# Performance work log

Measured on AMD Instinct MI355X. Metric: run time of the kernel, lower is better.

Reference implementation:

```python
import jax, jax.numpy as jnp
import numpy as np


def setup_inputs() -> dict:
    key = jax.random.key(0)
    k1, k2 = jax.random.split(key)
    B, C = 8192, 4096
    y_hat = jax.random.normal(k1, (B, C), dtype=jnp.float32)
    y = jax.random.randint(k2, (B, C), 0, 2).astype(jnp.float32)
    return {"y_hat": y_hat, "y": y}


def _bce_with_logits(x, y):
    # numerically stable mean BCE-with-logits (matches torch reduction='mean')
    return jnp.mean(jnp.maximum(x, 0.0) - x * y + jnp.log1p(jnp.exp(-jnp.abs(x))))


def _cross_label_dependency(x, y):
    # per-row: sum_{j: y=0, k: y!=0} exp(x_j - x_k) / (n0 * n1)
    # factorized: (sum_neg exp(x_j)) * (sum_pos exp(-x_k)) / (n0 * n1)
    pos = (y != 0.0)
    neg = jnp.logical_not(pos)
    s_neg = jnp.sum(jnp.where(neg, jnp.exp(x), 0.0), axis=1)   # [B]
    s_pos = jnp.sum(jnp.where(pos, jnp.exp(-x), 0.0), axis=1)  # [B]
    n0 = jnp.sum(neg, axis=1).astype(x.dtype)
    n1 = jnp.sum(pos, axis=1).astype(x.dtype)
    denom = n0 * n1
    per_row = jnp.where(denom > 0, s_neg * s_pos / jnp.maximum(denom, 1.0), 0.0)
    return jnp.mean(per_row)


def reference(y_hat, y):
    return _bce_with_logits(y_hat, y) + _cross_label_dependency(y_hat, y)
```

## Files before the change

### kernel.cpp

```cpp
#include <hip/hip_runtime.h>

#define B_ROWS 8192
#define C_COLS 4096

__device__ __forceinline__ float wave_reduce_sum(float v) {
    #pragma unroll
    for (int o = 32; o > 0; o >>= 1) v += __shfl_down(v, o, 64);
    return v;
}

__global__ __launch_bounds__(256) void row_stage(const float* __restrict__ x,
                                                 const float* __restrict__ y,
                                                 float* __restrict__ row_out) {
    const int row = blockIdx.x;
    const size_t base = (size_t)row * C_COLS;
    const float4* x4 = reinterpret_cast<const float4*>(x + base);
    const float4* y4 = reinterpret_cast<const float4*>(y + base);

    const float LOG2E  = 1.44269504088896340736f;
    const float N2LOG2E = -2.0f * 1.44269504088896340736f;
    const float LN2    = 0.69314718055994530942f;

    float s_neg = 0.f, s_pos = 0.f, bce = 0.f, n1 = 0.f;

    #pragma unroll
    for (int it = 0; it < 4; ++it) {
        const int i = it * 256 + threadIdx.x;
        float4 xv = x4[i];
        float4 yv = y4[i];
        float xs[4] = {xv.x, xv.y, xv.z, xv.w};
        float ys[4] = {yv.x, yv.y, yv.z, yv.w};
        float prod = 1.0f;
        #pragma unroll
        for (int k = 0; k < 4; ++k) {
            float xx = xs[k];
            float yy = ys[k];
            float m  = fmaf(N2LOG2E, yy, LOG2E);
            float eu = __builtin_amdgcn_exp2f(xx * m);
            s_pos = fmaf(yy,        eu, s_pos);
            s_neg = fmaf(1.0f - yy, eu, s_neg);
            n1   += yy;
            prod  = fmaf(prod, eu, prod);
        }
        bce = fmaf(LN2, __builtin_amdgcn_logf(prod), bce);
    }

    float a = wave_reduce_sum(s_neg);
    float b = wave_reduce_sum(s_pos);
    float c = wave_reduce_sum(bce);
    float d = wave_reduce_sum(n1);

    __shared__ float red[4][4];
    const int lane = threadIdx.x & 63;
    const int wid  = threadIdx.x >> 6;
    if (lane == 0) {
        red[wid][0] = a; red[wid][1] = b; red[wid][2] = c; red[wid][3] = d;
    }
    __syncthreads();

    if (threadIdx.x == 0) {
        float SN = red[0][0] + red[1][0] + red[2][0] + red[3][0];
        float SP = red[0][1] + red[1][1] + red[2][1] + red[3][1];
        float BC = red[0][2] + red[1][2] + red[2][2] + red[3][2];
        float N1 = red[0][3] + red[1][3] + red[2][3] + red[3][3];
        float N0 = (float)C_COLS - N1;
        float denom = N0 * N1;
        float per_row = (denom > 0.f) ? (SN * SP) / denom : 0.f;
        row_out[row] = BC * (1.0f / ((float)B_ROWS * (float)C_COLS))
                     + per_row * (1.0f / (float)B_ROWS);
    }
}

__global__ __launch_bounds__(256) void final_reduce(const float* __restrict__ row_vals,
                                                    float* __restrict__ out) {
    float s = 0.f;
    for (int i = threadIdx.x; i < B_ROWS; i += 256) s += row_vals[i];
    s = wave_reduce_sum(s);
    __shared__ float red[4];
    const int lane = threadIdx.x & 63;
    const int wid  = threadIdx.x >> 6;
    if (lane == 0) red[wid] = s;
    __syncthreads();
    if (threadIdx.x == 0) out[0] = red[0] + red[1] + red[2] + red[3];
}

extern "C" void kernel_launch(void* const* d_in, const int* in_sizes, int n_in,
                              void* d_out, int out_size, void* d_ws, size_t ws_size,
                              hipStream_t stream) {
    const float* x = (const float*)d_in[0];
    const float* y = (const float*)d_in[1];
    float* out = (float*)d_out;
    float* row_vals = (float*)d_ws;

    row_stage<<<B_ROWS, 256, 0, stream>>>(x, y, row_vals);
    final_reduce<<<1, 256, 0, stream>>>(row_vals, out);
}
```

Measured before the change: 50.82 us.

## Fuse final reduction via atomicAdd and hoist row loads ahead of compute

```diff
diff --git a/kernel.cpp b/kernel.cpp
--- a/kernel.cpp
+++ b/kernel.cpp
@@ -2,6 +2,8 @@
 
 #define B_ROWS 8192
 #define C_COLS 4096
+
+typedef float fv4 __attribute__((ext_vector_type(4)));
 
 __device__ __forceinline__ float wave_reduce_sum(float v) {
     #pragma unroll
@@ -11,41 +13,44 @@
 
 __global__ __launch_bounds__(256) void row_stage(const float* __restrict__ x,
                                                  const float* __restrict__ y,
-                                                 float* __restrict__ row_out) {
+                                                 float* __restrict__ out) {
     const int row = blockIdx.x;
     const size_t base = (size_t)row * C_COLS;
-    const float4* x4 = reinterpret_cast<const float4*>(x + base);
-    const float4* y4 = reinterpret_cast<const float4*>(y + base);
+    const fv4* x4 = reinterpret_cast<const fv4*>(x + base);
+    const fv4* y4 = reinterpret_cast<const fv4*>(y + base);
 
-    const float LOG2E  = 1.44269504088896340736f;
+    const float LOG2E   = 1.44269504088896340736f;
     const float N2LOG2E = -2.0f * 1.44269504088896340736f;
-    const float LN2    = 0.69314718055994530942f;
+    const float LN2     = 0.69314718055994530942f;
 
-    float s_neg = 0.f, s_pos = 0.f, bce = 0.f, n1 = 0.f;
+    fv4 xr[4], yr[4];
+    #pragma unroll
+    for (int it = 0; it < 4; ++it) {
+        const int i = it * 256 + threadIdx.x;
+        xr[it] = x4[i];
+        yr[it] = __builtin_nontemporal_load(&y4[i]);
+    }
+
+    float s_all = 0.f, s_pos = 0.f, bce = 0.f, n1 = 0.f;
 
     #pragma unroll
     for (int it = 0; it < 4; ++it) {
-        const int i = it * 256 + threadIdx.x;
-        float4 xv = x4[i];
-        float4 yv = y4[i];
-        float xs[4] = {xv.x, xv.y, xv.z, xv.w};
-        float ys[4] = {yv.x, yv.y, yv.z, yv.w};
         float prod = 1.0f;
         #pragma unroll
         for (int k = 0; k < 4; ++k) {
-            float xx = xs[k];
-            float yy = ys[k];
+            float xx = xr[it][k];
+            float yy = yr[it][k];
             float m  = fmaf(N2LOG2E, yy, LOG2E);
             float eu = __builtin_amdgcn_exp2f(xx * m);
-            s_pos = fmaf(yy,        eu, s_pos);
-            s_neg = fmaf(1.0f - yy, eu, s_neg);
+            s_all = s_all + eu;
+            s_pos = fmaf(yy, eu, s_pos);
             n1   += yy;
             prod  = fmaf(prod, eu, prod);
         }
         bce = fmaf(LN2, __builtin_amdgcn_logf(prod), bce);
     }
 
-    float a = wave_reduce_sum(s_neg);
+    float a = wave_reduce_sum(s_all);
     float b = wave_reduce_sum(s_pos);
     float c = wave_reduce_sum(bce);
     float d = wave_reduce_sum(n1);
@@ -59,29 +64,18 @@
     __syncthreads();
 
     if (threadIdx.x == 0) {
-        float SN = red[0][0] + red[1][0] + red[2][0] + red[3][0];
+        float SA = red[0][0] + red[1][0] + red[2][0] + red[3][0];
         float SP = red[0][1] + red[1][1] + red[2][1] + red[3][1];
         float BC = red[0][2] + red[1][2] + red[2][2] + red[3][2];
         float N1 = red[0][3] + red[1][3] + red[2][3] + red[3][3];
+        float SN = SA - SP;
         float N0 = (float)C_COLS - N1;
         float denom = N0 * N1;
         float per_row = (denom > 0.f) ? (SN * SP) / denom : 0.f;
-        row_out[row] = BC * (1.0f / ((float)B_ROWS * (float)C_COLS))
-                     + per_row * (1.0f / (float)B_ROWS);
+        float contrib = BC * (1.0f / ((float)B_ROWS * (float)C_COLS))
+                      + per_row * (1.0f / (float)B_ROWS);
+        atomicAdd(out, contrib);
     }
-}
-
-__global__ __launch_bounds__(256) void final_reduce(const float* __restrict__ row_vals,
-                                                    float* __restrict__ out) {
-    float s = 0.f;
-    for (int i = threadIdx.x; i < B_ROWS; i += 256) s += row_vals[i];
-    s = wave_reduce_sum(s);
-    __shared__ float red[4];
-    const int lane = threadIdx.x & 63;
-    const int wid  = threadIdx.x >> 6;
-    if (lane == 0) red[wid] = s;
-    __syncthreads();
-    if (threadIdx.x == 0) out[0] = red[0] + red[1] + red[2] + red[3];
 }
 
 extern "C" void kernel_launch(void* const* d_in, const int* in_sizes, int n_in,
@@ -90,8 +84,7 @@
     const float* x = (const float*)d_in[0];
     const float* y = (const float*)d_in[1];
     float* out = (float*)d_out;
-    float* row_vals = (float*)d_ws;
 
-    row_stage<<<B_ROWS, 256, 0, stream>>>(x, y, row_vals);
-    final_reduce<<<1, 256, 0, stream>>>(row_vals, out);
+    (void)hipMemsetAsync(out, 0, sizeof(float), stream);
+    row_stage<<<B_ROWS, 256, 0, stream>>>(x, y, out);
 }
```

Measured after the change: 121.7 us. 139% more time.
